# Performance work log

Hardware: AMD Instinct MI355X
Metric: run time of the kernel (lower is better)

## Reference

```python
import jax, jax.numpy as jnp
import numpy as np

N = 100000
E = 1600000
EPS = 1e-16
NEG_SLOPE = 0.2


def setup_inputs() -> dict:
    key = jax.random.key(0)
    ks = jax.random.split(key, 10)
    F_in, C = 512, 40
    H1, D1 = 8, 8
    return {
        "x": jax.random.normal(ks[0], (N, F_in), jnp.float32),
        "edge_index": jax.random.randint(ks[1], (2, E), 0, N, jnp.int64),
        "W1": jax.random.normal(ks[2], (F_in, H1 * D1), jnp.float32) * 0.05,
        "att_src1": jax.random.normal(ks[3], (H1, D1), jnp.float32) * 0.1,
        "att_dst1": jax.random.normal(ks[4], (H1, D1), jnp.float32) * 0.1,
        "b1": jnp.zeros((H1 * D1,), jnp.float32),
        "W2": jax.random.normal(ks[5], (H1 * D1, C), jnp.float32) * 0.05,
        "att_src2": jax.random.normal(ks[6], (1, C), jnp.float32) * 0.1,
        "att_dst2": jax.random.normal(ks[7], (1, C), jnp.float32) * 0.1,
        "b2": jnp.zeros((C,), jnp.float32),
    }


def gat_conv(x, W, att_src, att_dst, bias, src, dst, heads, out_dim, concat):
    # Linear transform per head: [N, H, D]
    h = (x @ W).reshape(N, heads, out_dim)
    # Per-node attention logits: [N, H]
    a_src = jnp.einsum("nhd,hd->nh", h, att_src)
    a_dst = jnp.einsum("nhd,hd->nh", h, att_dst)
    # Per-edge logits (edge j->i: src=j, softmax grouped by dst=i)
    e = a_src[src] + a_dst[dst]                      # [E', H]
    e = jax.nn.leaky_relu(e, NEG_SLOPE)
    # Segment softmax over destination nodes (numerically stable)
    m = jax.ops.segment_max(e, dst, num_segments=N)  # [N, H]
    e = jnp.exp(e - m[dst])
    s = jax.ops.segment_sum(e, dst, num_segments=N)  # [N, H]
    alpha = e / (s[dst] + EPS)                       # [E', H]
    # Weighted message aggregation (scatter-add)
    msg = h[src] * alpha[:, :, None]                 # [E', H, D]
    out = jax.ops.segment_sum(msg, dst, num_segments=N)  # [N, H, D]
    out = out.reshape(N, heads * out_dim) if concat else out.mean(axis=1)
    return out + bias


def reference(x, edge_index, W1, att_src1, att_dst1, b1, W2, att_src2, att_dst2, b2):
    # PyG GATConv default: add self-loops
    loops = jnp.arange(N, dtype=edge_index.dtype)
    src = jnp.concatenate([edge_index[0], loops])
    dst = jnp.concatenate([edge_index[1], loops])
    h = gat_conv(x, W1, att_src1, att_dst1, b1, src, dst, heads=8, out_dim=8, concat=True)
    h = jax.nn.elu(h)
    out = gat_conv(h, W2, att_src2, att_dst2, b2, src, dst, heads=1, out_dim=40, concat=False)
    return jax.nn.log_softmax(out, axis=1)
```

## Files before the change

kernel.cpp:

```cpp
#include <hip/hip_runtime.h>
#include <cstdint>

#define N_NODES 100000
#define N_EDGES 1600000
#define ETOT    1700000
#define FIN     512
#define HD1     64
#define C2      40
#define NEG_SLOPE 0.2f
#define GEMM1_NB 782
#define DEG_NB   832
#define SCAN_NB2 98

typedef __attribute__((ext_vector_type(8))) short bf16x8;
typedef __attribute__((ext_vector_type(4))) float f32x4;

__device__ __forceinline__ float lrelu(float v) { return v > 0.f ? v : NEG_SLOPE * v; }

__device__ __forceinline__ unsigned short f2bf(float f) {
    uint32_t u = __float_as_uint(f);
    u += 0x7FFF + ((u >> 16) & 1);
    return (unsigned short)(u >> 16);
}
__device__ __forceinline__ float bf2f(unsigned short u) {
    return __uint_as_float(((uint32_t)u) << 16);
}

__global__ void k_prep(const float* __restrict__ W1, const float* __restrict__ a_s,
                       const float* __restrict__ a_d,
                       const float* __restrict__ W2, const float* __restrict__ att_s2,
                       const float* __restrict__ att_d2,
                       unsigned short* __restrict__ W1t, unsigned short* __restrict__ W2t,
                       int* __restrict__ deg, unsigned int* __restrict__ flags) {
    int i = blockIdx.x * 256 + threadIdx.x;
    if (i < N_NODES) deg[i] = 0;
    if (i < 128) flags[i] = 0u;
    if (i < 80 * 512) {
        int n = i >> 9, k = i & 511;
        float v;
        if (n < 64) {
            v = W1[k * HD1 + n];
        } else if (n < 72) {
            int h = n - 64; v = 0.f;
#pragma unroll
            for (int d = 0; d < 8; d++) v += W1[k * HD1 + h * 8 + d] * a_s[h * 8 + d];
        } else {
            int h = n - 72; v = 0.f;
#pragma unroll
            for (int d = 0; d < 8; d++) v += W1[k * HD1 + h * 8 + d] * a_d[h * 8 + d];
        }
        W1t[n * FIN + k] = f2bf(v);
    } else if (i < 80 * 512 + 48 * 64) {
        int j = i - 80 * 512;
        int n = j >> 6, k = j & 63;
        float v = 0.f;
        if (n < C2) {
            v = W2[k * C2 + n];
        } else if (n == C2) {
            for (int c = 0; c < C2; c++) v += W2[k * C2 + c] * att_s2[c];
        } else if (n == C2 + 1) {
            for (int c = 0; c < C2; c++) v += W2[k * C2 + c] * att_d2[c];
        }
        W2t[n * 64 + k] = f2bf(v);
    }
}

__global__ __launch_bounds__(256) void k_g1deg(const float* __restrict__ x,
                                               const unsigned short* __restrict__ W1t,
                                               unsigned short* __restrict__ h1b,
                                               float* __restrict__ as1,
                                               float* __restrict__ ad1,
                                               const int* __restrict__ ei,
                                               int* __restrict__ deg,
                                               int* __restrict__ ord) {
    __shared__ unsigned short As[128 * 72];
    const int t = threadIdx.x;
    if (blockIdx.x >= GEMM1_NB) {
        for (int e = ((int)blockIdx.x - GEMM1_NB) * 256 + t; e < ETOT; e += DEG_NB * 256) {
            int dst = (e < N_EDGES) ? ei[N_EDGES + e] : e - N_EDGES;
            ord[e] = atomicAdd(&deg[dst], 1);
        }
        return;
    }
    const int lane = t & 63, wv = t >> 6;
    const int quad = lane >> 4, l16 = lane & 15;
    const int row0 = blockIdx.x * 128;

    f32x4 acc[2][5];
#pragma unroll
    for (int mi = 0; mi < 2; mi++)
#pragma unroll
        for (int ni = 0; ni < 5; ni++) acc[mi][ni] = (f32x4){0.f, 0.f, 0.f, 0.f};

    float4 rx[8];
#pragma unroll
    for (int i = 0; i < 8; i++) {
        int ff = t + i * 256;
        int r = ff >> 4, c4 = ff & 15;
        int row = row0 + r;
        rx[i] = (row < N_NODES) ? *(const float4*)&x[(size_t)row * FIN + c4 * 4]
                                : make_float4(0.f, 0.f, 0.f, 0.f);
    }

    for (int c = 0; c < 8; c++) {
#pragma unroll
        for (int i = 0; i < 8; i++) {
            int ff = t + i * 256;
            int r = ff >> 4, c4 = ff & 15;
            ushort4 s4;
            s4.x = f2bf(rx[i].x); s4.y = f2bf(rx[i].y);
            s4.z = f2bf(rx[i].z); s4.w = f2bf(rx[i].w);
            *(ushort4*)&As[r * 72 + c4 * 4] = s4;
        }
        __syncthreads();
        if (c < 7) {
            int kb = (c + 1) * 64;
#pragma unroll
            for (int i = 0; i < 8; i++) {
                int ff = t + i * 256;
                int r = ff >> 4, c4 = ff & 15;
                int row = row0 + r;
                rx[i] = (row < N_NODES) ? *(const float4*)&x[(size_t)row * FIN + kb + c4 * 4]
                                        : make_float4(0.f, 0.f, 0.f, 0.f);
            }
        }
        int kb = c * 64;
#pragma unroll
        for (int ks = 0; ks < 2; ks++) {
            bf16x8 af[2], bfv[5];
#pragma unroll
            for (int mi = 0; mi < 2; mi++) {
                int lr = wv * 32 + mi * 16 + l16;
                af[mi] = *(const bf16x8*)&As[lr * 72 + ks * 32 + quad * 8];
            }
#pragma unroll
            for (int ni = 0; ni < 5; ni++) {
                int n = ni * 16 + l16;
                bfv[ni] = *(const bf16x8*)&W1t[n * FIN + kb + ks * 32 + quad * 8];
            }
#pragma unroll
            for (int mi = 0; mi < 2; mi++)
#pragma unroll
                for (int ni = 0; ni < 5; ni++)
                    acc[mi][ni] = __builtin_amdgcn_mfma_f32_16x16x32_bf16(
                        af[mi], bfv[ni], acc[mi][ni], 0, 0, 0);
        }
        __syncthreads();
    }
#pragma unroll
    for (int mi = 0; mi < 2; mi++)
#pragma unroll
        for (int ni = 0; ni < 5; ni++)
#pragma unroll
            for (int r = 0; r < 4; r++) {
                int row = row0 + wv * 32 + mi * 16 + quad * 4 + r;
                if (row >= N_NODES) continue;
                int col = ni * 16 + l16;
                float v = acc[mi][ni][r];
                if (col < 64)       h1b[(size_t)row * 64 + col] = f2bf(v);
                else if (col < 72)  as1[row * 8 + (col - 64)] = v;
                else                ad1[row * 8 + (col - 72)] = v;
            }
}

__global__ __launch_bounds__(1024) void k_scan_lb(const int* __restrict__ deg,
                                                  int* __restrict__ row_ptr,
                                                  int* __restrict__ aggr,
                                                  int* __restrict__ incl,
                                                  unsigned int* __restrict__ flags) {
    __shared__ int sh[1024];
    __shared__ int shbase;
    const int t = threadIdx.x, b = blockIdx.x;
    const int i = b * 1024 + t;
    int v = (i < N_NODES) ? deg[i] : 0;
    sh[t] = v;
    __syncthreads();
    for (int off = 1; off < 1024; off <<= 1) {
        int u = (t >= off) ? sh[t - off] : 0;
        __syncthreads();
        sh[t] += u;
        __syncthreads();
    }
    if (t == 0) {
        int total = sh[1023];
        int run = 0;
        if (b == 0) {
            __hip_atomic_store(&incl[0], total, __ATOMIC_RELEASE, __HIP_MEMORY_SCOPE_AGENT);
            __hip_atomic_store(&flags[0], 2u, __ATOMIC_RELEASE, __HIP_MEMORY_SCOPE_AGENT);
        } else {
            __hip_atomic_store(&aggr[b], total, __ATOMIC_RELEASE, __HIP_MEMORY_SCOPE_AGENT);
            __hip_atomic_store(&flags[b], 1u, __ATOMIC_RELEASE, __HIP_MEMORY_SCOPE_AGENT);
            int p = b - 1;
            while (true) {
                unsigned int f = __hip_atomic_load(&flags[p], __ATOMIC_ACQUIRE,
                                                   __HIP_MEMORY_SCOPE_AGENT);
                if (f == 2u) {
                    run += __hip_atomic_load(&incl[p], __ATOMIC_ACQUIRE,
                                             __HIP_MEMORY_SCOPE_AGENT);
                    break;
                } else if (f == 1u) {
                    run += __hip_atomic_load(&aggr[p], __ATOMIC_ACQUIRE,
                                             __HIP_MEMORY_SCOPE_AGENT);
                    --p;
                }
            }
            __hip_atomic_store(&incl[b], run + total, __ATOMIC_RELEASE,
                               __HIP_MEMORY_SCOPE_AGENT);
            __hip_atomic_store(&flags[b], 2u, __ATOMIC_RELEASE, __HIP_MEMORY_SCOPE_AGENT);
        }
        shbase = run;
        if (b == 0) row_ptr[N_NODES] = ETOT;
    }
    __syncthreads();
    int base = shbase;
    if (i < N_NODES) row_ptr[i] = base + sh[t] - v;
}

__global__ void k_scatter(const int* __restrict__ ei, const int* __restrict__ row_ptr,
                          const int* __restrict__ ord, int* __restrict__ csr_src) {
    int e = blockIdx.x * 256 + threadIdx.x;
    if (e >= ETOT) return;
    int src, dst;
    if (e < N_EDGES) { src = ei[e]; dst = ei[N_EDGES + e]; }
    else             { src = dst = e - N_EDGES; }
    csr_src[row_ptr[dst] + ord[e]] = src;
}

__global__ __launch_bounds__(256) void k_agg1(
    const unsigned short* __restrict__ h1b,
    const float* __restrict__ as1, const float* __restrict__ ad1,
    const int* __restrict__ row_ptr, const int* __restrict__ csr_src,
    const float* __restrict__ b1, unsigned short* __restrict__ hb) {
    int t = threadIdx.x, wv = t >> 6, lane = t & 63;
    int dst = blockIdx.x * 4 + wv;
    if (dst >= N_NODES) return;
    int g = lane >> 3, i8 = lane & 7;
    int s0 = row_ptr[dst], s1e = row_ptr[dst + 1];
    float adh = ad1[dst * 8 + i8];
    float den = 0.f;
    float facc[8];
#pragma unroll
    for (int d = 0; d < 8; d++) facc[d] = 0.f;

    for (int base = s0; base < s1e; base += 64) {
        int idx = base + lane;
        int sl = (idx < s1e) ? csr_src[idx] : 0;
        int cnt = min(64, s1e - base);
        for (int j = 0; j < cnt; j += 16) {
            int sA = __shfl(sl, j + g);
            int sB = __shfl(sl, j + 8 + g);
            bool vA = (j + g) < cnt, vB = (j + 8 + g) < cnt;
            bf16x8 rA = *(const bf16x8*)&h1b[(size_t)sA * 64 + i8 * 8];
            bf16x8 rB = *(const bf16x8*)&h1b[(size_t)sB * 64 + i8 * 8];
            float aA = as1[sA * 8 + i8];
            float aB = as1[sB * 8 + i8];
            float wA = vA ? __expf(lrelu(aA + adh)) : 0.f;
            float wB = vB ? __expf(lrelu(aB + adh)) : 0.f;
            den += wA + wB;
#pragma unroll
            for (int d = 0; d < 8; d++)
                facc[d] += wA * bf2f((unsigned short)rA[d]) +
                           wB * bf2f((unsigned short)rB[d]);
        }
    }
#pragma unroll
    for (int o = 8; o <= 32; o <<= 1) {
        den += __shfl_xor(den, o, 64);
#pragma unroll
        for (int d = 0; d < 8; d++) facc[d] += __shfl_xor(facc[d], o, 64);
    }
    float rden = 1.f / (den + 1e-16f);
    float4 b1lo = *(const float4*)&b1[i8 * 8];
    float4 b1hi = *(const float4*)&b1[i8 * 8 + 4];
    float bb[8] = {b1lo.x, b1lo.y, b1lo.z, b1lo.w, b1hi.x, b1hi.y, b1hi.z, b1hi.w};
    bf16x8 pk;
#pragma unroll
    for (int d = 0; d < 8; d++) {
        float hv = facc[d] * rden + bb[d];
        hv = hv > 0.f ? hv : expm1f(hv);
        pk[d] = (short)f2bf(hv);
    }
    if (g == 0) *(bf16x8*)&hb[(size_t)dst * 64 + i8 * 8] = pk;
}

__global__ __launch_bounds__(256) void k_gemm2(const unsigned short* __restrict__ hb,
                                               const unsigned short* __restrict__ W2t,
                                               unsigned short* __restrict__ h2b,
                                               float* __restrict__ as2,
                                               float* __restrict__ ad2) {
    const int t = threadIdx.x;
    const int lane = t & 63, wv = t >> 6;
    const int quad = lane >> 4, l16 = lane & 15;
    const int row0 = blockIdx.x * 128;

    f32x4 acc[2][3];
#pragma unroll
    for (int mi = 0; mi < 2; mi++)
#pragma unroll
        for (int ni = 0; ni < 3; ni++) acc[mi][ni] = (f32x4){0.f, 0.f, 0.f, 0.f};

    bf16x8 bfrag[2][3];
#pragma unroll
    for (int ks = 0; ks < 2; ks++)
#pragma unroll
        for (int ni = 0; ni < 3; ni++)
            bfrag[ks][ni] = *(const bf16x8*)&W2t[(ni * 16 + l16) * 64 + ks * 32 + quad * 8];

#pragma unroll
    for (int mi = 0; mi < 2; mi++) {
        int row = row0 + wv * 32 + mi * 16 + l16;
        int rowc = row < N_NODES ? row : N_NODES - 1;
#pragma unroll
        for (int ks = 0; ks < 2; ks++) {
            bf16x8 af = *(const bf16x8*)&hb[(size_t)rowc * 64 + ks * 32 + quad * 8];
#pragma unroll
            for (int ni = 0; ni < 3; ni++)
                acc[mi][ni] = __builtin_amdgcn_mfma_f32_16x16x32_bf16(
                    af, bfrag[ks][ni], acc[mi][ni], 0, 0, 0);
        }
    }
#pragma unroll
    for (int mi = 0; mi < 2; mi++)
#pragma unroll
        for (int ni = 0; ni < 3; ni++)
#pragma unroll
            for (int r = 0; r < 4; r++) {
                int row = row0 + wv * 32 + mi * 16 + quad * 4 + r;
                if (row >= N_NODES) continue;
                int col = ni * 16 + l16;
                float v = acc[mi][ni][r];
                if (col < C2)            h2b[(size_t)row * C2 + col] = f2bf(v);
                else if (col == C2)      as2[row] = v;
                else if (col == C2 + 1)  ad2[row] = v;
            }
}

__global__ __launch_bounds__(256) void k_agg2(
    const unsigned short* __restrict__ h2b,
    const float* __restrict__ as2, const float* __restrict__ ad2,
    const int* __restrict__ row_ptr, const int* __restrict__ csr_src,
    const float* __restrict__ b2, float* __restrict__ out) {
    int t = threadIdx.x, wv = t >> 6, lane = t & 63;
    int dst = blockIdx.x * 4 + wv;
    if (dst >= N_NODES) return;
    int g = lane >> 3, i8 = lane & 7;
    bool act = i8 < 5;
    int off = act ? i8 * 8 : 0;
    int s0 = row_ptr[dst], s1e = row_ptr[dst + 1];
    float ad = ad2[dst];
    float denp = 0.f;
    float facc[8];
#pragma unroll
    for (int d = 0; d < 8; d++) facc[d] = 0.f;

    for (int base = s0; base < s1e; base += 64) {
        int idx = base + lane;
        int sl = (idx < s1e) ? csr_src[idx] : 0;
        int cnt = min(64, s1e - base);
        for (int j = 0; j < cnt; j += 16) {
            int sA = __shfl(sl, j + g);
            int sB = __shfl(sl, j + 8 + g);
            bool vA = (j + g) < cnt, vB = (j + 8 + g) < cnt;
            bf16x8 rA = *(const bf16x8*)&h2b[(size_t)sA * C2 + off];
            bf16x8 rB = *(const bf16x8*)&h2b[(size_t)sB * C2 + off];
            float aA = as2[sA];
            float aB = as2[sB];
            float wfA = vA ? __expf(lrelu(aA + ad)) : 0.f;
            float wfB = vB ? __expf(lrelu(aB + ad)) : 0.f;
            if (i8 == 0) denp += wfA + wfB;
            float wA = act ? wfA : 0.f;
            float wB = act ? wfB : 0.f;
#pragma unroll
            for (int d = 0; d < 8; d++)
                facc[d] += wA * bf2f((unsigned short)rA[d]) +
                           wB * bf2f((unsigned short)rB[d]);
        }
    }
#pragma unroll
    for (int o = 8; o <= 32; o <<= 1)
#pragma unroll
        for (int d = 0; d < 8; d++) facc[d] += __shfl_xor(facc[d], o, 64);
    float den = denp;
#pragma unroll
    for (int o = 32; o >= 1; o >>= 1) den += __shfl_xor(den, o, 64);
    float rden = 1.f / (den + 1e-16f);

    float vch[8];
    float mx = -1e30f;
#pragma unroll
    for (int d = 0; d < 8; d++) {
        vch[d] = act ? facc[d] * rden + b2[off + d] : -1e30f;
        mx = fmaxf(mx, vch[d]);
    }
#pragma unroll
    for (int o = 1; o <= 4; o <<= 1) mx = fmaxf(mx, __shfl_xor(mx, o, 64));
    float es = 0.f;
#pragma unroll
    for (int d = 0; d < 8; d++) es += act ? __expf(vch[d] - mx) : 0.f;
#pragma unroll
    for (int o = 1; o <= 4; o <<= 1) es += __shfl_xor(es, o, 64);
    float lg = logf(es);
    if (g == 0 && act) {
        float4 o0 = {vch[0] - mx - lg, vch[1] - mx - lg, vch[2] - mx - lg, vch[3] - mx - lg};
        float4 o1 = {vch[4] - mx - lg, vch[5] - mx - lg, vch[6] - mx - lg, vch[7] - mx - lg};
        *(float4*)&out[(size_t)dst * C2 + i8 * 8]     = o0;
        *(float4*)&out[(size_t)dst * C2 + i8 * 8 + 4] = o1;
    }
}

extern "C" void kernel_launch(void* const* d_in, const int* in_sizes, int n_in,
                              void* d_out, int out_size, void* d_ws, size_t ws_size,
                              hipStream_t stream) {
    const float* x     = (const float*)d_in[0];
    const int*   ei    = (const int*)d_in[1];
    const float* W1    = (const float*)d_in[2];
    const float* at_s1 = (const float*)d_in[3];
    const float* at_d1 = (const float*)d_in[4];
    const float* b1    = (const float*)d_in[5];
    const float* W2    = (const float*)d_in[6];
    const float* at_s2 = (const float*)d_in[7];
    const float* at_d2 = (const float*)d_in[8];
    const float* b2    = (const float*)d_in[9];
    float* out = (float*)d_out;
    float* ws  = (float*)d_ws;

    unsigned short* h1b = (unsigned short*)ws;
    float* as1 = ws + 3200000;
    float* ad1 = ws + 4000000;
    unsigned short* hb  = (unsigned short*)(ws + 4800000);
    unsigned short* h2b = (unsigned short*)(ws + 8000000);
    float* as2 = ws + 10000000;
    float* ad2 = ws + 10100000;
    unsigned short* W1t = (unsigned short*)(ws + 10200000);
    unsigned short* W2t = (unsigned short*)(ws + 10250000);
    int* row_ptr = (int*)(ws + 10300000);
    int* deg     = (int*)(ws + 10410000);
    int* csr_src = (int*)(ws + 10630000);
    int* aggrA   = (int*)(ws + 12340000);
    int* inclA   = (int*)(ws + 12350000);
    unsigned int* flags = (unsigned int*)(ws + 12360000);
    int* ord     = (int*)(ws + 13000000);

    k_prep<<<391, 256, 0, stream>>>(W1, at_s1, at_d1, W2, at_s2, at_d2, W1t, W2t, deg, flags);
    k_g1deg<<<GEMM1_NB + DEG_NB, 256, 0, stream>>>(x, W1t, h1b, as1, ad1, ei, deg, ord);
    k_scan_lb<<<SCAN_NB2, 1024, 0, stream>>>(deg, row_ptr, aggrA, inclA, flags);
    k_scatter<<<(ETOT + 255) / 256, 256, 0, stream>>>(ei, row_ptr, ord, csr_src);
    k_agg1<<<(N_NODES + 3) / 4, 256, 0, stream>>>(h1b, as1, ad1, row_ptr, csr_src, b1, hb);
    k_gemm2<<<(N_NODES + 127) / 128, 256, 0, stream>>>(hb, W2t, h2b, as2, ad2);
    k_agg2<<<(N_NODES + 3) / 4, 256, 0, stream>>>(h2b, as2, ad2, row_ptr, csr_src, b2, out);
}
```

Before: 565.7 us.

## Fuse layer-2 linear transform into layer-1 aggregation; reorder degree blocks first

The second GEMM (64x42 projection plus attention logits) is folded into the layer-1 aggregation kernel. Each wavefront multiplies its aggregated, ELU-activated row by W2, which is staged in shared memory as fp32, and the hb intermediate and the separate k_gemm2 launch go away. The degree-counting blocks now occupy the low block indices and their count drops from 832 to 480, so the atomics are scheduled ahead of the GEMM blocks. The fused path uses scalar FMAs and shuffles instead of MFMA, and each block pays for a shared-memory load of W2 before it starts.

```diff
diff --git a/kernel.cpp b/kernel.cpp
--- a/kernel.cpp
+++ b/kernel.cpp
@@ -8,8 +8,8 @@
 #define HD1     64
 #define C2      40
 #define NEG_SLOPE 0.2f
+#define DEG_NB   480
 #define GEMM1_NB 782
-#define DEG_NB   832
 #define SCAN_NB2 98
 
 typedef __attribute__((ext_vector_type(8))) short bf16x8;
@@ -75,8 +75,8 @@
                                                int* __restrict__ ord) {
     __shared__ unsigned short As[128 * 72];
     const int t = threadIdx.x;
-    if (blockIdx.x >= GEMM1_NB) {
-        for (int e = ((int)blockIdx.x - GEMM1_NB) * 256 + t; e < ETOT; e += DEG_NB * 256) {
+    if (blockIdx.x < DEG_NB) {
+        for (int e = (int)blockIdx.x * 256 + t; e < ETOT; e += DEG_NB * 256) {
             int dst = (e < N_EDGES) ? ei[N_EDGES + e] : e - N_EDGES;
             ord[e] = atomicAdd(&deg[dst], 1);
         }
@@ -84,7 +84,7 @@
     }
     const int lane = t & 63, wv = t >> 6;
     const int quad = lane >> 4, l16 = lane & 15;
-    const int row0 = blockIdx.x * 128;
+    const int row0 = ((int)blockIdx.x - DEG_NB) * 128;
 
     f32x4 acc[2][5];
 #pragma unroll
@@ -226,14 +226,22 @@
     csr_src[row_ptr[dst] + ord[e]] = src;
 }
 
-__global__ __launch_bounds__(256) void k_agg1(
+__global__ __launch_bounds__(256) void k_agg1f(
     const unsigned short* __restrict__ h1b,
     const float* __restrict__ as1, const float* __restrict__ ad1,
     const int* __restrict__ row_ptr, const int* __restrict__ csr_src,
-    const float* __restrict__ b1, unsigned short* __restrict__ hb) {
+    const float* __restrict__ b1, const unsigned short* __restrict__ W2t,
+    unsigned short* __restrict__ h2b, float* __restrict__ as2,
+    float* __restrict__ ad2) {
+    __shared__ float w2l[64][48];
     int t = threadIdx.x, wv = t >> 6, lane = t & 63;
+    for (int i = t; i < 64 * 48; i += 256) {
+        int k = i / 48, c = i - k * 48;
+        w2l[k][c] = bf2f(W2t[c * 64 + k]);
+    }
+    __syncthreads();
+
     int dst = blockIdx.x * 4 + wv;
-    if (dst >= N_NODES) return;
     int g = lane >> 3, i8 = lane & 7;
     int s0 = row_ptr[dst], s1e = row_ptr[dst + 1];
     float adh = ad1[dst * 8 + i8];
@@ -273,66 +281,25 @@
     float4 b1lo = *(const float4*)&b1[i8 * 8];
     float4 b1hi = *(const float4*)&b1[i8 * 8 + 4];
     float bb[8] = {b1lo.x, b1lo.y, b1lo.z, b1lo.w, b1hi.x, b1hi.y, b1hi.z, b1hi.w};
-    bf16x8 pk;
+    float hv[8];
 #pragma unroll
     for (int d = 0; d < 8; d++) {
-        float hv = facc[d] * rden + bb[d];
-        hv = hv > 0.f ? hv : expm1f(hv);
-        pk[d] = (short)f2bf(hv);
-    }
-    if (g == 0) *(bf16x8*)&hb[(size_t)dst * 64 + i8 * 8] = pk;
-}
-
-__global__ __launch_bounds__(256) void k_gemm2(const unsigned short* __restrict__ hb,
-                                               const unsigned short* __restrict__ W2t,
-                                               unsigned short* __restrict__ h2b,
-                                               float* __restrict__ as2,
-                                               float* __restrict__ ad2) {
-    const int t = threadIdx.x;
-    const int lane = t & 63, wv = t >> 6;
-    const int quad = lane >> 4, l16 = lane & 15;
-    const int row0 = blockIdx.x * 128;
-
-    f32x4 acc[2][3];
-#pragma unroll
-    for (int mi = 0; mi < 2; mi++)
-#pragma unroll
-        for (int ni = 0; ni < 3; ni++) acc[mi][ni] = (f32x4){0.f, 0.f, 0.f, 0.f};
-
-    bf16x8 bfrag[2][3];
-#pragma unroll
-    for (int ks = 0; ks < 2; ks++)
-#pragma unroll
-        for (int ni = 0; ni < 3; ni++)
-            bfrag[ks][ni] = *(const bf16x8*)&W2t[(ni * 16 + l16) * 64 + ks * 32 + quad * 8];
-
-#pragma unroll
-    for (int mi = 0; mi < 2; mi++) {
-        int row = row0 + wv * 32 + mi * 16 + l16;
-        int rowc = row < N_NODES ? row : N_NODES - 1;
-#pragma unroll
-        for (int ks = 0; ks < 2; ks++) {
-            bf16x8 af = *(const bf16x8*)&hb[(size_t)rowc * 64 + ks * 32 + quad * 8];
-#pragma unroll
-            for (int ni = 0; ni < 3; ni++)
-                acc[mi][ni] = __builtin_amdgcn_mfma_f32_16x16x32_bf16(
-                    af, bfrag[ks][ni], acc[mi][ni], 0, 0, 0);
-        }
-    }
-#pragma unroll
-    for (int mi = 0; mi < 2; mi++)
-#pragma unroll
-        for (int ni = 0; ni < 3; ni++)
-#pragma unroll
-            for (int r = 0; r < 4; r++) {
-                int row = row0 + wv * 32 + mi * 16 + quad * 4 + r;
-                if (row >= N_NODES) continue;
-                int col = ni * 16 + l16;
-                float v = acc[mi][ni][r];
-                if (col < C2)            h2b[(size_t)row * C2 + col] = f2bf(v);
-                else if (col == C2)      as2[row] = v;
-                else if (col == C2 + 1)  ad2[row] = v;
-            }
+        float v = facc[d] * rden + bb[d];
+        hv[d] = v > 0.f ? v : expm1f(v);
+    }
+    int cidx = lane < 48 ? lane : 0;
+    float out = 0.f;
+#pragma unroll
+    for (int ks = 0; ks < 8; ks++) {
+#pragma unroll
+        for (int d = 0; d < 8; d++) {
+            float hk = __shfl(hv[d], ks);
+            out += hk * w2l[ks * 8 + d][cidx];
+        }
+    }
+    if (lane < C2)            h2b[(size_t)dst * C2 + lane] = f2bf(out);
+    else if (lane == C2)      as2[dst] = out;
+    else if (lane == C2 + 1)  ad2[dst] = out;
 }
 
 __global__ __launch_bounds__(256) void k_agg2(
@@ -427,7 +394,6 @@
     unsigned short* h1b = (unsigned short*)ws;
     float* as1 = ws + 3200000;
     float* ad1 = ws + 4000000;
-    unsigned short* hb  = (unsigned short*)(ws + 4800000);
     unsigned short* h2b = (unsigned short*)(ws + 8000000);
     float* as2 = ws + 10000000;
     float* ad2 = ws + 10100000;
@@ -442,10 +408,10 @@
     int* ord     = (int*)(ws + 13000000);
 
     k_prep<<<391, 256, 0, stream>>>(W1, at_s1, at_d1, W2, at_s2, at_d2, W1t, W2t, deg, flags);
-    k_g1deg<<<GEMM1_NB + DEG_NB, 256, 0, stream>>>(x, W1t, h1b, as1, ad1, ei, deg, ord);
+    k_g1deg<<<DEG_NB + GEMM1_NB, 256, 0, stream>>>(x, W1t, h1b, as1, ad1, ei, deg, ord);
     k_scan_lb<<<SCAN_NB2, 1024, 0, stream>>>(deg, row_ptr, aggrA, inclA, flags);
     k_scatter<<<(ETOT + 255) / 256, 256, 0, stream>>>(ei, row_ptr, ord, csr_src);
-    k_agg1<<<(N_NODES + 3) / 4, 256, 0, stream>>>(h1b, as1, ad1, row_ptr, csr_src, b1, hb);
-    k_gemm2<<<(N_NODES + 127) / 128, 256, 0, stream>>>(hb, W2t, h2b, as2, ad2);
+    k_agg1f<<<N_NODES / 4, 256, 0, stream>>>(h1b, as1, ad1, row_ptr, csr_src, b1, W2t,
+                                             h2b, as2, ad2);
     k_agg2<<<(N_NODES + 3) / 4, 256, 0, stream>>>(h2b, as2, ad2, row_ptr, csr_src, b2, out);
 }
```

After: 722.7 us. 1.28x slower.
